# Kernel tuning notes

Measured on AMD Instinct MI355X. Metric: run time of the kernel, lower is better.

## Reference

```python
import jax, jax.numpy as jnp
import numpy as np

# ---- module config (init_kwargs) ----
B, CIN, H, W_ = 2, 64, 56, 56
COUT, KH, KW = 128, 3, 3
K = CIN * KH * KW               # 576, reduction dim
ARRAY_ROWS = 128
IN_SLICES = (2, 2, 2, 2)        # 8-bit inputs, 2-bit slices
W_SLICES = (2, 2, 2, 2)         # 8-bit weights, 2-bit slices
N_STEPS_IN = 2 ** sum(IN_SLICES)    # 256, unsigned quantizer
N_STEPS_W = 2 ** sum(W_SLICES)      # 256
ADC_BINS = 256
ADC_STEP = 4.0

def _shifts_masks(slices):
    masks, shifts = [], [0]
    for s in slices[::-1]:
        masks.append((1 << s) - 1)
        shifts.append(s + shifts[-1])
    return np.array(shifts[-2::-1], np.int32), np.array(masks[::-1], np.int32)

_ish, _im = _shifts_masks(IN_SLICES)
_wsh, _wm = _shifts_masks(W_SLICES)
ISH, IM = jnp.asarray(_ish), jnp.asarray(_im)
WSH, WM = jnp.asarray(_wsh), jnp.asarray(_wm)
ISF = jnp.asarray((1 << _ish).astype(np.float32))  # slice recombine weights 2^shift
WSF = jnp.asarray((1 << _wsh).astype(np.float32))


def setup_inputs() -> dict:
    key = jax.random.key(0)
    k1, k2 = jax.random.split(key)
    return {
        "x": jax.random.normal(k1, (B, CIN, H, W_), jnp.float32),
        "w": jax.random.normal(k2, (COUT, CIN, KH, KW), jnp.float32),
    }


def _im2col(x):
    # 3x3 SAME conv patches, ordering [Cin, kh, kw] to match w.reshape(COUT, K)
    xp = jnp.pad(x, ((0, 0), (0, 0), (1, 1), (1, 1)))
    cols = jnp.stack([xp[:, :, i:i + H, j:j + W_]
                      for i in range(KH) for j in range(KW)], axis=2)  # [B,Cin,9,H,W]
    return cols.transpose(0, 3, 4, 1, 2).reshape(B * H * W_, K)  # [Nx, K]


def _quant_unsigned(v, n_steps):
    # Quantizer.offset + Quantizer.forward (unsigned, per-row over dim=-1)
    offs = v.min(axis=-1, keepdims=True)
    vr = v - offs
    step = vr.max(axis=-1, keepdims=True) / (n_steps - 1)
    q = jnp.round(jnp.clip(vr, 0.0, step * n_steps) / step).astype(jnp.int32)
    return q, step[..., 0], offs[..., 0]


def _slice_bits(q, shifts, masks):
    # Slicer.forward: stack (q >> shift) & mask along new leading slice dim
    s = shifts.reshape((-1,) + (1,) * q.ndim)
    m = masks.reshape((-1,) + (1,) * q.ndim)
    return (q[None] >> s) & m


def _chunk(t):
    # Chunker.forward over last dim K
    nb = -(-K // ARRAY_ROWS)
    npb = -(-K // nb)
    pad = nb * npb - K
    t = jnp.pad(t, [(0, 0)] * (t.ndim - 1) + [(0, pad)])
    t = t.reshape(t.shape[:-1] + (nb, npb))
    return jnp.moveaxis(t, -2, 0)  # [nb, ..., npb]


def reference(x, w):
    xf = _im2col(x)                    # [Nx, K]
    wf = w.reshape(COUT, K)            # [Ny, K]
    x_sum = xf.sum(axis=-1)            # [Nx]
    w_sum = wf.sum(axis=-1)            # [Ny]

    xq, x_scale, x_offs = _quant_unsigned(xf, N_STEPS_IN)
    wq, w_scale, w_offs = _quant_unsigned(wf, N_STEPS_W)

    xc = _chunk(_slice_bits(xq, ISH, IM))  # [nb, nis, Nx, npb] int32
    wc = _chunk(_slice_bits(wq, WSH, WM))  # [nb, nws, Ny, npb] int32

    # bit-serial crossbar MACs per (chunk, weight-slice, input-slice)
    z = jnp.einsum('bixk,bwyk->bwixy',
                   xc.astype(jnp.float32), wc.astype(jnp.float32))  # [nb,nws,nis,Nx,Ny]

    # ADC digitization (unsigned, fixed step): quantize then dequantize
    z = jnp.round(jnp.clip(z, 0.0, ADC_STEP * ADC_BINS) / ADC_STEP) * ADC_STEP

    # Chunker.reverse: sum crossbar blocks; Slicer.reverse: shift-weighted sums
    z = z.sum(axis=0)                               # [nws,nis,Nx,Ny]
    z = jnp.einsum('wixy,w,i->xy', z, WSF, ISF)     # [Nx,Ny]

    # dequantize scales and unsigned-offset correction:
    # x.y = sx*sy*(xq.yq) + x_offs*sum(y) + y_offs*sum(x) - x_offs*y_offs*K
    z = z * x_scale[:, None] * w_scale[None, :]
    z = (z + x_offs[:, None] * w_sum[None, :]
           + w_offs[None, :] * x_sum[:, None]
           - x_offs[:, None] * w_offs[None, :] * K)

    return z.reshape(B, H, W_, COUT).transpose(0, 3, 1, 2)  # [B,Cout,H,W]
```

## Files before the change

### kernel.cpp

```cpp
#include <hip/hip_runtime.h>


#define NX    6272
#define NY    128
#define KDIM  576
#define NCH   5
#define NPB   116
#define RT    392
#define CTN   8

typedef int i32x4 __attribute__((ext_vector_type(4)));

__device__ __forceinline__ int frag_off(int chunk, int tile, int ntile,
                                        int kk, int rowInTile) {
    int ks   = kk >> 6;
    int lgrp = (kk >> 4) & 3;
    int j    = kk & 15;
    int ln   = lgrp * 16 + rowInTile;
    return (((chunk * ntile + tile) * 2 + ks) * 64 + ln) * 16 + j;
}

__device__ __forceinline__ int stg_off(int chunk, int kk, int rl) {
    int ks   = kk >> 6;
    int lgrp = (kk >> 4) & 3;
    int j    = kk & 15;
    return (chunk * 2 + ks) * 1024 + (lgrp * 16 + rl) * 16 + j;
}

__device__ __forceinline__ i32x4 slice2b(i32x4 v, int sh) {
    i32x4 r;
    r[0] = (int)(((unsigned)v[0] >> sh) & 0x03030303u);
    r[1] = (int)(((unsigned)v[1] >> sh) & 0x03030303u);
    r[2] = (int)(((unsigned)v[2] >> sh) & 0x03030303u);
    r[3] = (int)(((unsigned)v[3] >> sh) & 0x03030303u);
    return r;
}

__global__ __launch_bounds__(256) void k_quant(
    const float* __restrict__ x, const float* __restrict__ w,
    unsigned char* __restrict__ Xq, unsigned char* __restrict__ Wq,
    float* __restrict__ x_scale, float* __restrict__ x_offs, float* __restrict__ x_sum,
    float* __restrict__ w_scale, float* __restrict__ w_offs, float* __restrict__ w_sum)
{
    __shared__ float xs2[64 * 57];
    __shared__ __align__(16) unsigned char stg[10240];

    int rtile = blockIdx.x;
    int b = rtile >= 196 ? 1 : 0;
    int prt = rtile - b * 196;
    int pos0 = prt * 16;
    const float* xb = x + (size_t)(b * 64) * 3136;

    for (int i = threadIdx.x; i < 64 * 54; i += 256) {
        int cin = i / 54, rem = i - cin * 54;
        int kh = rem / 18;
        int g = pos0 + (rem - kh * 18) - 1;
        float vv = 0.f;
        if (g >= 0 && g < 3136) {
            int hg = g / 56, wg = g - hg * 56;
            int r = hg - 1 + kh;
            if (r >= 0 && r < 56) vv = xb[cin * 3136 + r * 56 + wg];
        }
        xs2[cin * 57 + rem] = vv;
    }
    __syncthreads();

    int wave = threadIdx.x >> 6, lane = threadIdx.x & 63;
#pragma unroll
    for (int qi = 0; qi < 4; qi++) {
        int i = wave * 4 + qi;
        int pos = pos0 + i;
        int w_ = pos - (pos / 56) * 56;
        float v[9];
#pragma unroll
        for (int kh = 0; kh < 3; kh++)
#pragma unroll
            for (int kw = 0; kw < 3; kw++) {
                int ww = w_ - 1 + kw;
                v[kh * 3 + kw] = (ww >= 0 && ww < 56)
                               ? xs2[lane * 57 + kh * 18 + i + kw] : 0.f;
            }
        float mn = v[0], mx = v[0], sm = 0.f;
#pragma unroll
        for (int r = 0; r < 9; r++) { mn = fminf(mn, v[r]); mx = fmaxf(mx, v[r]); sm += v[r]; }
#pragma unroll
        for (int off = 32; off > 0; off >>= 1) {
            mn = fminf(mn, __shfl_xor(mn, off));
            mx = fmaxf(mx, __shfl_xor(mx, off));
            sm += __shfl_xor(sm, off);
        }
        float step = (mx - mn) / 255.0f;
        int xrow = rtile * 16 + i;
        if (lane == 0) { x_scale[xrow] = step; x_offs[xrow] = mn; x_sum[xrow] = sm; }
#pragma unroll
        for (int r = 0; r < 9; r++) {
            int t2 = lane * 9 + r;
            int q = (int)rintf((v[r] - mn) / step);
            q = q < 0 ? 0 : (q > 255 ? 255 : q);
            int chunk = t2 / NPB, kk = t2 - chunk * NPB;
            stg[stg_off(chunk, kk, i)] = (unsigned char)q;
        }
        {
            int chunk, kk;
            if (lane < 48) { chunk = lane / 12; kk = NPB + lane % 12; }
            else           { chunk = 4;        kk = 112 + (lane - 48); }
            stg[stg_off(chunk, kk, i)] = 0;
        }
    }
    __syncthreads();

    for (int idx = threadIdx.x; idx < 640; idx += 256) {
        int c = idx >> 7, off = (idx & 127) * 16;
        *(i32x4*)(Xq + (size_t)(c * RT + rtile) * 2048 + off) =
            *(const i32x4*)(stg + c * 2048 + off);
    }

    if (rtile < NY && wave == 0) {
        int row = rtile;
        const float* wr = w + row * KDIM;
        float v[9];
#pragma unroll
        for (int r = 0; r < 9; r++) v[r] = wr[lane * 9 + r];
        float mn = v[0], mx = v[0], sm = 0.f;
#pragma unroll
        for (int r = 0; r < 9; r++) { mn = fminf(mn, v[r]); mx = fmaxf(mx, v[r]); sm += v[r]; }
#pragma unroll
        for (int off = 32; off > 0; off >>= 1) {
            mn = fminf(mn, __shfl_xor(mn, off));
            mx = fmaxf(mx, __shfl_xor(mx, off));
            sm += __shfl_xor(sm, off);
        }
        float step = (mx - mn) / 255.0f;
        if (lane == 0) { w_scale[row] = step; w_offs[row] = mn; w_sum[row] = sm; }
        int ctile = row >> 4, rl = row & 15;
#pragma unroll
        for (int r = 0; r < 9; r++) {
            int t2 = lane * 9 + r;
            int q = (int)rintf((v[r] - mn) / step);
            q = q < 0 ? 0 : (q > 255 ? 255 : q);
            int chunk = t2 / NPB, kk = t2 - chunk * NPB;
            Wq[frag_off(chunk, ctile, CTN, kk, rl)] = (unsigned char)q;
        }
        int chunk, kk;
        if (lane < 48) { chunk = lane / 12; kk = NPB + lane % 12; }
        else           { chunk = 4;        kk = 112 + (lane - 48); }
        Wq[frag_off(chunk, ctile, CTN, kk, rl)] = 0;
    }
}

__global__ __launch_bounds__(256) void k_main(
    const unsigned char* __restrict__ Xq, const unsigned char* __restrict__ Wq,
    const float* __restrict__ x_scale, const float* __restrict__ x_offs,
    const float* __restrict__ x_sum,
    const float* __restrict__ w_scale, const float* __restrict__ w_offs,
    const float* __restrict__ w_sum,
    float* __restrict__ out)
{
    int wid   = blockIdx.x * 4 + (threadIdx.x >> 6);
    int rtile = wid >> 3;
    int ctile = wid & 7;
    int lane  = threadIdx.x & 63;

    i32x4 acc = {0, 0, 0, 0};
    const i32x4 zero = {0, 0, 0, 0};

    for (int chunk = 0; chunk < NCH; chunk++) {
        const i32x4* Ab = (const i32x4*)(Xq + ((chunk * RT + rtile) * 2 * 64 + lane) * 16);
        const i32x4* Bb = (const i32x4*)(Wq + ((chunk * CTN + ctile) * 2 * 64 + lane) * 16);
        i32x4 ar0 = Ab[0], ar1 = Ab[64];
        i32x4 br0 = Bb[0], br1 = Bb[64];

        i32x4 ws_sl[4][2];
#pragma unroll
        for (int ws = 0; ws < 4; ws++) {
            ws_sl[ws][0] = slice2b(br0, 6 - 2 * ws);
            ws_sl[ws][1] = slice2b(br1, 6 - 2 * ws);
        }
#pragma unroll
        for (int is = 0; is < 4; is++) {
            int ish = 6 - 2 * is;
            i32x4 b0 = slice2b(ar0, ish);
            i32x4 b1 = slice2b(ar1, ish);
#pragma unroll
            for (int ws = 0; ws < 4; ws++) {
                i32x4 d = __builtin_amdgcn_mfma_i32_16x16x64_i8(ws_sl[ws][0], b0, zero, 0, 0, 0);
                d = __builtin_amdgcn_mfma_i32_16x16x64_i8(ws_sl[ws][1], b1, d, 0, 0, 0);
                int sh = ish + (6 - 2 * ws);
#pragma unroll
                for (int r = 0; r < 4; r++) {
                    int z = d[r];
                    z = z > 1024 ? 1024 : z;
                    int r4 = (z + 1 + ((z >> 2) & 1)) & ~3;
                    acc[r] += r4 << sh;
                }
            }
        }
    }

    int cl = lane & 15, g = lane >> 4;
    int xrow = rtile * 16 + cl;
    float xs = x_scale[xrow], xo = x_offs[xrow], xsm = x_sum[xrow];
    int bb = rtile >= 196 ? 1 : 0;
    int hw = xrow - bb * 3136;
#pragma unroll
    for (int r = 0; r < 4; r++) {
        int wrow = ctile * 16 + g * 4 + r;
        float tt = ((float)acc[r] * xs) * w_scale[wrow];
        float res = ((tt + xo * w_sum[wrow]) + w_offs[wrow] * xsm)
                  - (xo * w_offs[wrow]) * 576.0f;
        out[(bb * 128 + wrow) * 3136 + hw] = res;
    }
}

extern "C" void kernel_launch(void* const* d_in, const int* in_sizes, int n_in,
                              void* d_out, int out_size, void* d_ws, size_t ws_size,
                              hipStream_t stream) {
    const float* x = (const float*)d_in[0];
    const float* w = (const float*)d_in[1];
    float* out = (float*)d_out;

    unsigned char* Xq = (unsigned char*)d_ws;
    unsigned char* Wq = Xq + 5 * RT * 2048;
    float* x_scale = (float*)(Wq + 5 * CTN * 2048);
    float* x_offs  = x_scale + NX;
    float* x_sum   = x_offs + NX;
    float* w_scale = x_sum + NX;
    float* w_offs  = w_scale + NY;
    float* w_sum   = w_offs + NY;

    hipLaunchKernelGGL(k_quant, dim3(RT), dim3(256), 0, stream,
                       x, w, Xq, Wq, x_scale, x_offs, x_sum, w_scale, w_offs, w_sum);
    hipLaunchKernelGGL(k_main, dim3(784), dim3(256), 0, stream,
                       Xq, Wq, x_scale, x_offs, x_sum, w_scale, w_offs, w_sum, out);
}
```

Baseline: 38.14 us.

## Fuse quantization and bit-sliced MFMA matmul into one kernel using LDS staging

Merges the quantize kernel and the main MFMA kernel into a single 1024-thread kernel. Each block quantizes 32 input rows into LDS and recomputes the full 128-row weight quantization locally, then runs the bit-sliced MFMA from LDS. This removes the global round trip for the quantized operands and scale vectors, plus one kernel launch. In exchange every block repeats the weight quantization, the grid shrinks to 196 large blocks using about 128KB of LDS, which limits occupancy, and a hipFuncSetAttribute call runs on every launch.

```diff
diff --git a/kernel.cpp b/kernel.cpp
--- a/kernel.cpp
+++ b/kernel.cpp
@@ -6,19 +6,8 @@
 #define KDIM  576
 #define NCH   5
 #define NPB   116
-#define RT    392
-#define CTN   8
 
 typedef int i32x4 __attribute__((ext_vector_type(4)));
-
-__device__ __forceinline__ int frag_off(int chunk, int tile, int ntile,
-                                        int kk, int rowInTile) {
-    int ks   = kk >> 6;
-    int lgrp = (kk >> 4) & 3;
-    int j    = kk & 15;
-    int ln   = lgrp * 16 + rowInTile;
-    return (((chunk * ntile + tile) * 2 + ks) * 64 + ln) * 16 + j;
-}
 
 __device__ __forceinline__ int stg_off(int chunk, int kk, int rl) {
     int ks   = kk >> 6;
@@ -36,40 +25,75 @@
     return r;
 }
 
-__global__ __launch_bounds__(256) void k_quant(
+__device__ __forceinline__ void rowstats(float (&v)[9], float& step,
+                                         float& mn_, float& sm_) {
+    float mn = v[0], mx = v[0], sm = 0.f;
+#pragma unroll
+    for (int r = 0; r < 9; r++) { mn = fminf(mn, v[r]); mx = fmaxf(mx, v[r]); sm += v[r]; }
+#pragma unroll
+    for (int off = 32; off > 0; off >>= 1) {
+        mn = fminf(mn, __shfl_xor(mn, off));
+        mx = fmaxf(mx, __shfl_xor(mx, off));
+        sm += __shfl_xor(sm, off);
+    }
+    step = (mx - mn) / 255.0f;
+    mn_ = mn; sm_ = sm;
+}
+
+__device__ __forceinline__ void scatter_row(unsigned char* stg, float (&v)[9],
+                                            float mn, float step, int rl, int lane) {
+#pragma unroll
+    for (int r = 0; r < 9; r++) {
+        int t2 = lane * 9 + r;
+        int q = (int)rintf((v[r] - mn) / step);
+        q = q < 0 ? 0 : (q > 255 ? 255 : q);
+        int chunk = t2 / NPB, kk = t2 - chunk * NPB;
+        stg[stg_off(chunk, kk, rl)] = (unsigned char)q;
+    }
+    int chunk, kk;
+    if (lane < 48) { chunk = lane / 12; kk = NPB + lane % 12; }
+    else           { chunk = 4;        kk = 112 + (lane - 48); }
+    stg[stg_off(chunk, kk, rl)] = 0;
+}
+
+extern __shared__ unsigned char lds[];
+
+__global__ __launch_bounds__(1024) void k_all(
     const float* __restrict__ x, const float* __restrict__ w,
-    unsigned char* __restrict__ Xq, unsigned char* __restrict__ Wq,
-    float* __restrict__ x_scale, float* __restrict__ x_offs, float* __restrict__ x_sum,
-    float* __restrict__ w_scale, float* __restrict__ w_offs, float* __restrict__ w_sum)
+    float* __restrict__ out)
 {
-    __shared__ float xs2[64 * 57];
-    __shared__ __align__(16) unsigned char stg[10240];
+    unsigned char* stgW = lds;
+    unsigned char* stgX = lds + 81920;
+    float* xsc = (float*)(lds + 102400);
+    float* xof = xsc + 32;  float* xsm = xof + 32;
+    float* wsc = xsm + 32;  float* wof = wsc + 128;  float* wsm = wof + 128;
+    float* xs2 = (float*)(lds + 104320);
 
-    int rtile = blockIdx.x;
-    int b = rtile >= 196 ? 1 : 0;
-    int prt = rtile - b * 196;
-    int pos0 = prt * 16;
+    int blk = blockIdx.x;
+    int tid = threadIdx.x;
+    int wv = tid >> 6, lane = tid & 63;
+    int b = blk >= 98 ? 1 : 0;
+    int pos_base = (blk - 98 * b) * 32;
     const float* xb = x + (size_t)(b * 64) * 3136;
 
-    for (int i = threadIdx.x; i < 64 * 54; i += 256) {
-        int cin = i / 54, rem = i - cin * 54;
-        int kh = rem / 18;
-        int g = pos0 + (rem - kh * 18) - 1;
+    for (int i = tid; i < 64 * 102; i += 1024) {
+        int cin = i / 102, rem = i - cin * 102;
+        int kh = rem / 34, c = rem - kh * 34;
+        int g = pos_base + c - 1;
         float vv = 0.f;
         if (g >= 0 && g < 3136) {
             int hg = g / 56, wg = g - hg * 56;
             int r = hg - 1 + kh;
             if (r >= 0 && r < 56) vv = xb[cin * 3136 + r * 56 + wg];
         }
-        xs2[cin * 57 + rem] = vv;
+        xs2[cin * 103 + rem] = vv;
     }
     __syncthreads();
 
-    int wave = threadIdx.x >> 6, lane = threadIdx.x & 63;
 #pragma unroll
-    for (int qi = 0; qi < 4; qi++) {
-        int i = wave * 4 + qi;
-        int pos = pos0 + i;
+    for (int qi = 0; qi < 2; qi++) {
+        int i = wv * 2 + qi;
+        int pos = pos_base + i;
         int w_ = pos - (pos / 56) * 56;
         float v[9];
 #pragma unroll
@@ -78,97 +102,40 @@
             for (int kw = 0; kw < 3; kw++) {
                 int ww = w_ - 1 + kw;
                 v[kh * 3 + kw] = (ww >= 0 && ww < 56)
-                               ? xs2[lane * 57 + kh * 18 + i + kw] : 0.f;
+                               ? xs2[lane * 103 + kh * 34 + i + kw] : 0.f;
             }
-        float mn = v[0], mx = v[0], sm = 0.f;
-#pragma unroll
-        for (int r = 0; r < 9; r++) { mn = fminf(mn, v[r]); mx = fmaxf(mx, v[r]); sm += v[r]; }
-#pragma unroll
-        for (int off = 32; off > 0; off >>= 1) {
-            mn = fminf(mn, __shfl_xor(mn, off));
-            mx = fmaxf(mx, __shfl_xor(mx, off));
-            sm += __shfl_xor(sm, off);
-        }
-        float step = (mx - mn) / 255.0f;
-        int xrow = rtile * 16 + i;
-        if (lane == 0) { x_scale[xrow] = step; x_offs[xrow] = mn; x_sum[xrow] = sm; }
-#pragma unroll
-        for (int r = 0; r < 9; r++) {
-            int t2 = lane * 9 + r;
-            int q = (int)rintf((v[r] - mn) / step);
-            q = q < 0 ? 0 : (q > 255 ? 255 : q);
-            int chunk = t2 / NPB, kk = t2 - chunk * NPB;
-            stg[stg_off(chunk, kk, i)] = (unsigned char)q;
-        }
-        {
-            int chunk, kk;
-            if (lane < 48) { chunk = lane / 12; kk = NPB + lane % 12; }
-            else           { chunk = 4;        kk = 112 + (lane - 48); }
-            stg[stg_off(chunk, kk, i)] = 0;
-        }
-    }
-    __syncthreads();
-
-    for (int idx = threadIdx.x; idx < 640; idx += 256) {
-        int c = idx >> 7, off = (idx & 127) * 16;
-        *(i32x4*)(Xq + (size_t)(c * RT + rtile) * 2048 + off) =
-            *(const i32x4*)(stg + c * 2048 + off);
+        float step, mn, sm;
+        rowstats(v, step, mn, sm);
+        if (lane == 0) { xsc[i] = step; xof[i] = mn; xsm[i] = sm; }
+        scatter_row(stgX + (i >> 4) * 10240, v, mn, step, i & 15, lane);
     }
 
-    if (rtile < NY && wave == 0) {
-        int row = rtile;
+#pragma unroll
+    for (int qi = 0; qi < 8; qi++) {
+        int row = wv * 8 + qi;
         const float* wr = w + row * KDIM;
         float v[9];
 #pragma unroll
         for (int r = 0; r < 9; r++) v[r] = wr[lane * 9 + r];
-        float mn = v[0], mx = v[0], sm = 0.f;
-#pragma unroll
-        for (int r = 0; r < 9; r++) { mn = fminf(mn, v[r]); mx = fmaxf(mx, v[r]); sm += v[r]; }
-#pragma unroll
-        for (int off = 32; off > 0; off >>= 1) {
-            mn = fminf(mn, __shfl_xor(mn, off));
-            mx = fmaxf(mx, __shfl_xor(mx, off));
-            sm += __shfl_xor(sm, off);
-        }
-        float step = (mx - mn) / 255.0f;
-        if (lane == 0) { w_scale[row] = step; w_offs[row] = mn; w_sum[row] = sm; }
-        int ctile = row >> 4, rl = row & 15;
-#pragma unroll
-        for (int r = 0; r < 9; r++) {
-            int t2 = lane * 9 + r;
-            int q = (int)rintf((v[r] - mn) / step);
-            q = q < 0 ? 0 : (q > 255 ? 255 : q);
-            int chunk = t2 / NPB, kk = t2 - chunk * NPB;
-            Wq[frag_off(chunk, ctile, CTN, kk, rl)] = (unsigned char)q;
-        }
-        int chunk, kk;
-        if (lane < 48) { chunk = lane / 12; kk = NPB + lane % 12; }
-        else           { chunk = 4;        kk = 112 + (lane - 48); }
-        Wq[frag_off(chunk, ctile, CTN, kk, rl)] = 0;
+        float step, mn, sm;
+        rowstats(v, step, mn, sm);
+        if (lane == 0) { wsc[row] = step; wof[row] = mn; wsm[row] = sm; }
+        scatter_row(stgW + (row >> 4) * 10240, v, mn, step, row & 15, lane);
     }
-}
+    __syncthreads();
 
-__global__ __launch_bounds__(256) void k_main(
-    const unsigned char* __restrict__ Xq, const unsigned char* __restrict__ Wq,
-    const float* __restrict__ x_scale, const float* __restrict__ x_offs,
-    const float* __restrict__ x_sum,
-    const float* __restrict__ w_scale, const float* __restrict__ w_offs,
-    const float* __restrict__ w_sum,
-    float* __restrict__ out)
-{
-    int wid   = blockIdx.x * 4 + (threadIdx.x >> 6);
-    int rtile = wid >> 3;
-    int ctile = wid & 7;
-    int lane  = threadIdx.x & 63;
+    int rt = wv >> 3, ctl = wv & 7;
+    const unsigned char* Wb = stgW + ctl * 10240;
+    const unsigned char* Xb = stgX + rt * 10240;
 
     i32x4 acc = {0, 0, 0, 0};
     const i32x4 zero = {0, 0, 0, 0};
 
     for (int chunk = 0; chunk < NCH; chunk++) {
-        const i32x4* Ab = (const i32x4*)(Xq + ((chunk * RT + rtile) * 2 * 64 + lane) * 16);
-        const i32x4* Bb = (const i32x4*)(Wq + ((chunk * CTN + ctile) * 2 * 64 + lane) * 16);
-        i32x4 ar0 = Ab[0], ar1 = Ab[64];
-        i32x4 br0 = Bb[0], br1 = Bb[64];
+        const i32x4* Ax = (const i32x4*)(Xb + chunk * 2048 + lane * 16);
+        const i32x4* Aw = (const i32x4*)(Wb + chunk * 2048 + lane * 16);
+        i32x4 ar0 = Ax[0], ar1 = Ax[64];
+        i32x4 br0 = Aw[0], br1 = Aw[64];
 
         i32x4 ws_sl[4][2];
 #pragma unroll
@@ -198,17 +165,16 @@
     }
 
     int cl = lane & 15, g = lane >> 4;
-    int xrow = rtile * 16 + cl;
-    float xs = x_scale[xrow], xo = x_offs[xrow], xsm = x_sum[xrow];
-    int bb = rtile >= 196 ? 1 : 0;
-    int hw = xrow - bb * 3136;
+    int i_loc = rt * 16 + cl;
+    float xs = xsc[i_loc], xo = xof[i_loc], xsmv = xsm[i_loc];
+    int hw = pos_base + i_loc;
 #pragma unroll
     for (int r = 0; r < 4; r++) {
-        int wrow = ctile * 16 + g * 4 + r;
-        float tt = ((float)acc[r] * xs) * w_scale[wrow];
-        float res = ((tt + xo * w_sum[wrow]) + w_offs[wrow] * xsm)
-                  - (xo * w_offs[wrow]) * 576.0f;
-        out[(bb * 128 + wrow) * 3136 + hw] = res;
+        int wrow = ctl * 16 + g * 4 + r;
+        float tt = ((float)acc[r] * xs) * wsc[wrow];
+        float res = ((tt + xo * wsm[wrow]) + wof[wrow] * xsmv)
+                  - (xo * wof[wrow]) * 576.0f;
+        out[(b * 128 + wrow) * 3136 + hw] = res;
     }
 }
 
@@ -219,17 +185,8 @@
     const float* w = (const float*)d_in[1];
     float* out = (float*)d_out;
 
-    unsigned char* Xq = (unsigned char*)d_ws;
-    unsigned char* Wq = Xq + 5 * RT * 2048;
-    float* x_scale = (float*)(Wq + 5 * CTN * 2048);
-    float* x_offs  = x_scale + NX;
-    float* x_sum   = x_offs + NX;
-    float* w_scale = x_sum + NX;
-    float* w_offs  = w_scale + NY;
-    float* w_sum   = w_offs + NY;
+    (void)hipFuncSetAttribute((const void*)k_all,
+                              hipFuncAttributeMaxDynamicSharedMemorySize, 130688);
 
-    hipLaunchKernelGGL(k_quant, dim3(RT), dim3(256), 0, stream,
-                       x, w, Xq, Wq, x_scale, x_offs, x_sum, w_scale, w_offs, w_sum);
-    hipLaunchKernelGGL(k_main, dim3(784), dim3(256), 0, stream,
-                       Xq, Wq, x_scale, x_offs, x_sum, w_scale, w_offs, w_sum, out);
+    hipLaunchKernelGGL(k_all, dim3(196), dim3(1024), 130688, stream, x, w, out);
 }
```

After: 47.93 us. 25.7% more time.
